# Performance work log

Measured on AMD Instinct MI355X. Metric: run time of the kernel, lower is better.

## Reference

```python
import jax, jax.numpy as jnp
import numpy as np

D_MODEL = 256
D_STATE = 16
D_INNER = 512          # expand=2 * d_model
D_CONV = 4
DT_RANK = 16           # ceil(d_model/16)
B, L = 16, 2048


def setup_inputs() -> dict:
    key = jax.random.key(0)
    ks = jax.random.split(key, 10)
    s = 0.02
    inp = {
        "x": jax.random.normal(ks[0], (B, L, D_MODEL), dtype=jnp.float32),
        "ln_w": jnp.ones((D_MODEL,), jnp.float32),
        "ln_b": jnp.zeros((D_MODEL,), jnp.float32),
        "in_proj_w": jax.random.normal(ks[1], (2 * D_INNER, D_MODEL)) * s,
        "conv_w": jax.random.normal(ks[2], (D_INNER, 1, D_CONV)) * s,
        "conv_b": jnp.zeros((D_INNER,), jnp.float32),
        "x_proj_w": jax.random.normal(ks[3], (DT_RANK + 2 * D_STATE, D_INNER)) * s,
        "dt_proj_w": jax.random.normal(ks[4], (D_INNER, DT_RANK)) * s,
        "dt_proj_b": jax.random.uniform(ks[5], (D_INNER,), minval=-4.0, maxval=-2.0),
        "A_log": jnp.log(jnp.broadcast_to(jnp.arange(1, D_STATE + 1, dtype=jnp.float32), (D_INNER, D_STATE))).copy(),
        "D_param": jnp.ones((D_INNER,), jnp.float32),
        "out_proj_w": jax.random.normal(ks[6], (D_MODEL, D_INNER)) * s,
    }
    return inp


def _layernorm(x, w, b, eps=1e-5):
    mu = jnp.mean(x, axis=-1, keepdims=True)
    var = jnp.var(x, axis=-1, keepdims=True)
    return (x - mu) * jax.lax.rsqrt(var + eps) * w + b


def _mamba(xn, in_proj_w, conv_w, conv_b, x_proj_w, dt_proj_w, dt_proj_b, A_log, D_param, out_proj_w):
    # in_proj -> x, z   (B, L, d_inner) each
    xz = jnp.einsum('bld,ed->ble', xn, in_proj_w)
    x_in, z = jnp.split(xz, 2, axis=-1)

    # depthwise causal conv over L
    xc = jax.lax.conv_general_dilated(
        jnp.transpose(x_in, (0, 2, 1)), conv_w,
        window_strides=(1,), padding=[(D_CONV - 1, 0)],
        feature_group_count=D_INNER,
        dimension_numbers=('NCH', 'OIH', 'NCH')) + conv_b[None, :, None]
    xc = jax.nn.silu(jnp.transpose(xc, (0, 2, 1)))  # (B, L, d_inner)

    # input-dependent dt, B, C
    dbc = jnp.einsum('ble,fe->blf', xc, x_proj_w)  # (B, L, dt_rank + 2N)
    dt = jax.nn.softplus(jnp.einsum('blr,er->ble', dbc[..., :DT_RANK], dt_proj_w) + dt_proj_b)
    Bc = dbc[..., DT_RANK:DT_RANK + D_STATE]   # (B, L, N)
    Cc = dbc[..., DT_RANK + D_STATE:]          # (B, L, N)

    A = -jnp.exp(A_log)  # (d_inner, N)

    def step(h, inputs):
        dt_t, x_t, B_t, C_t = inputs  # (B,e), (B,e), (B,n), (B,n)
        dA = jnp.exp(dt_t[..., None] * A)                      # (B, e, n)
        h = dA * h + dt_t[..., None] * B_t[:, None, :] * x_t[..., None]
        y = jnp.sum(h * C_t[:, None, :], axis=-1)              # (B, e)
        return h, y

    h0 = jnp.zeros((xn.shape[0], D_INNER, D_STATE), xn.dtype)
    seq = (jnp.swapaxes(dt, 0, 1), jnp.swapaxes(xc, 0, 1),
           jnp.swapaxes(Bc, 0, 1), jnp.swapaxes(Cc, 0, 1))
    _, ys = jax.lax.scan(step, h0, seq)
    y = jnp.swapaxes(ys, 0, 1) + D_param * xc                  # (B, L, e)
    y = y * jax.nn.silu(z)
    return jnp.einsum('ble,de->bld', y, out_proj_w)


def reference(x, ln_w, ln_b, in_proj_w, conv_w, conv_b, x_proj_w, dt_proj_w, dt_proj_b, A_log, D_param, out_proj_w):
    xn = _layernorm(x, ln_w, ln_b)
    out = _mamba(xn, in_proj_w, conv_w, conv_b, x_proj_w, dt_proj_w, dt_proj_b, A_log, D_param, out_proj_w)
    return x + out  # dropout is identity in eval
```

## Files before the change

kernel.cpp:

```cpp
#include <hip/hip_runtime.h>
#include <cstdint>

#define DEVI __device__ __forceinline__

typedef __bf16 bf16;
typedef __bf16 bf16x8 __attribute__((ext_vector_type(8)));
typedef __bf16 bf16x4 __attribute__((ext_vector_type(4)));
typedef __bf16 bf16x2 __attribute__((ext_vector_type(2)));
typedef float floatx4 __attribute__((ext_vector_type(4)));
typedef float f32x2 __attribute__((ext_vector_type(2)));

constexpr int BATCH = 16, SEQ = 2048, DM = 256, DI = 512;
constexpr int M = BATCH * SEQ;
constexpr int NC = 128;
constexpr int CL = SEQ / NC;
static_assert(NC * CL == SEQ, "chunking");
constexpr float LOG2E = 1.4426950408889634f;

DEVI void gl2lds16(const void* g, void* l) {
  __builtin_amdgcn_global_load_lds(
      (const __attribute__((address_space(1))) unsigned int*)(uintptr_t)g,
      (__attribute__((address_space(3))) unsigned int*)(unsigned int)(uintptr_t)l,
      16, 0, 0);
}

DEVI float sigmoidf_(float x) { return 1.f / (1.f + __expf(-x)); }
DEVI float exp2_(float x) { return __builtin_amdgcn_exp2f(x); }

DEVI float bflo(unsigned u) { return __uint_as_float(u << 16); }
DEVI float bfhi(unsigned u) { return __uint_as_float(u & 0xFFFF0000u); }
DEVI f32x2 sp2(float v) { f32x2 r; r[0] = v; r[1] = v; return r; }

DEVI void powseq(f32x2 d, f32x2* P) {
  P[0] = d;
  P[1] = d * d;
  P[2] = P[1] * d;
  P[3] = P[1] * P[1];
  P[4] = P[3] * d;
  P[5] = P[3] * P[1];
  P[6] = P[3] * P[2];
  P[7] = P[3] * P[3];
  P[8] = P[7] * d;
  P[9] = P[7] * P[1];
  P[10] = P[7] * P[2];
  P[11] = P[7] * P[3];
  P[12] = P[7] * P[4];
  P[13] = P[7] * P[5];
  P[14] = P[7] * P[6];
  P[15] = P[7] * P[7];
}

__global__ __launch_bounds__(256) void prep_kernel(
    const float* __restrict__ w1, const float* __restrict__ wx,
    const float* __restrict__ wo, const float* __restrict__ alog,
    bf16* __restrict__ w1b, bf16* __restrict__ wxb, bf16* __restrict__ wob,
    float* __restrict__ An, int* __restrict__ flags) {
  constexpr int n1 = 1024 * 256, n2 = 48 * 512, n3 = 256 * 512;
  int i = blockIdx.x * 256 + threadIdx.x;
  if (i < n1) w1b[i] = (bf16)w1[i];
  else if (i < n1 + n2) wxb[i - n1] = (bf16)wx[i - n1];
  else if (i < n1 + n2 + n3) wob[i - n1 - n2] = (bf16)wo[i - n1 - n2];
  else if (i < n1 + n2 + n3 + DI) {
    const int e = i - (n1 + n2 + n3);
    const float a0 = -__expf(alog[e * 16]);
    bool ok = (a0 < 0.f);
#pragma unroll 1
    for (int s = 0; s < 16; s++) {
      const float a = -__expf(alog[e * 16 + s]);
      An[e * 16 + s] = a * LOG2E;
      ok = ok && (__builtin_fabsf(a / a0 - (float)(s + 1)) < 1e-3f);
    }
    flags[e] = ok ? 1 : 0;
  }
}

__global__ __launch_bounds__(256) void ln_kernel(
    const float* __restrict__ x, const float* __restrict__ w,
    const float* __restrict__ b, bf16* __restrict__ xn) {
  const int row = blockIdx.x * 4 + (threadIdx.x >> 6);
  const int lane = threadIdx.x & 63;
  const float4 v = ((const float4*)(x + (size_t)row * DM))[lane];
  float s = v.x + v.y + v.z + v.w;
  float s2 = v.x * v.x + v.y * v.y + v.z * v.z + v.w * v.w;
#pragma unroll
  for (int m = 1; m < 64; m <<= 1) { s += __shfl_xor(s, m); s2 += __shfl_xor(s2, m); }
  const float mu = s * (1.f / DM);
  const float var = s2 * (1.f / DM) - mu * mu;
  const float rs = rsqrtf(var + 1e-5f);
  const float4 wv = ((const float4*)w)[lane];
  const float4 bv = ((const float4*)b)[lane];
  bf16x4 o;
  o[0] = (bf16)((v.x - mu) * rs * wv.x + bv.x);
  o[1] = (bf16)((v.y - mu) * rs * wv.y + bv.y);
  o[2] = (bf16)((v.z - mu) * rs * wv.z + bv.z);
  o[3] = (bf16)((v.w - mu) * rs * wv.w + bv.w);
  *(bf16x4*)(xn + (size_t)row * DM + lane * 4) = o;
}

template <int N, int K, bool OUT_BF16, bool RESID>
__global__ __launch_bounds__(256) void gemm_nt(const bf16* __restrict__ A,
                                               const bf16* __restrict__ W,
                                               void* __restrict__ out,
                                               const float* __restrict__ resid) {
  constexpr int BK = 32;
  constexpr int NB = N / 128;
  constexpr int MT_PER = (M / 128) / 8;
  __shared__ __align__(16) bf16 lA[128 * BK];
  __shared__ __align__(16) bf16 lB[128 * BK];
  const int tid = threadIdx.x;
  const int id = blockIdx.x;
  const int xcd = id & 7;
  const int local = id >> 3;
  const int bm = (xcd * MT_PER + local / NB) * 128;
  const int bn = (local % NB) * 128;
  const int wave = tid >> 6, lane = tid & 63;
  const int wm = (wave >> 1) * 64, wn = (wave & 1) * 64;
  const int q = lane >> 4, r = lane & 15;
  floatx4 acc[4][4] = {};
  const int c0 = wave * 64 + lane;
  const int row0 = c0 >> 2, kp = (c0 & 3) * 8;
  for (int k0 = 0; k0 < K; k0 += BK) {
    gl2lds16(A + (size_t)(bm + row0) * K + k0 + kp, lA + c0 * 8);
    gl2lds16(A + (size_t)(bm + row0 + 64) * K + k0 + kp, lA + (c0 + 256) * 8);
    gl2lds16(W + (size_t)(bn + row0) * K + k0 + kp, lB + c0 * 8);
    gl2lds16(W + (size_t)(bn + row0 + 64) * K + k0 + kp, lB + (c0 + 256) * 8);
    __syncthreads();
    bf16x8 af[4], bfr[4];
#pragma unroll
    for (int i = 0; i < 4; i++) af[i] = *(const bf16x8*)&lA[(wm + i * 16 + r) * BK + q * 8];
#pragma unroll
    for (int j = 0; j < 4; j++) bfr[j] = *(const bf16x8*)&lB[(wn + j * 16 + r) * BK + q * 8];
#pragma unroll
    for (int i = 0; i < 4; i++)
#pragma unroll
      for (int j = 0; j < 4; j++)
        acc[i][j] = __builtin_amdgcn_mfma_f32_16x16x32_bf16(af[i], bfr[j], acc[i][j], 0, 0, 0);
    __syncthreads();
  }
#pragma unroll
  for (int i = 0; i < 4; i++)
#pragma unroll
    for (int j = 0; j < 4; j++)
#pragma unroll
      for (int t = 0; t < 4; t++) {
        const int row = bm + wm + i * 16 + q * 4 + t;
        const int col = bn + wn + j * 16 + r;
        const size_t idx = (size_t)row * N + col;
        float v = acc[i][j][t];
        if constexpr (OUT_BF16) {
          ((bf16*)out)[idx] = (bf16)v;
        } else {
          if constexpr (RESID) v += resid[idx];
          ((float*)out)[idx] = v;
        }
      }
}

__global__ __launch_bounds__(256) void conv_silu(const bf16* __restrict__ xz,
                                                 const float* __restrict__ cw,
                                                 const float* __restrict__ cb,
                                                 bf16* __restrict__ xc) {
  const int tid = threadIdx.x;
  const int e2 = tid * 2;
  const int p0 = blockIdx.x * 8;
  const int b = blockIdx.y;
  const float4 w0 = ((const float4*)cw)[e2];
  const float4 w1 = ((const float4*)cw)[e2 + 1];
  const float2 bias = *(const float2*)(cb + e2);
  float xa[11], xb_[11];
#pragma unroll
  for (int j = 0; j < 11; j++) {
    const int pos = p0 - 3 + j;
    float fa = 0.f, fb = 0.f;
    if (pos >= 0) {
      const unsigned u = *(const unsigned*)(xz + ((size_t)b * SEQ + pos) * 1024 + e2);
      fa = __uint_as_float(u << 16);
      fb = __uint_as_float(u & 0xFFFF0000u);
    }
    xa[j] = fa; xb_[j] = fb;
  }
#pragma unroll
  for (int k = 0; k < 8; k++) {
    const float a0 = bias.x + xa[k] * w0.x + xa[k + 1] * w0.y + xa[k + 2] * w0.z + xa[k + 3] * w0.w;
    const float a1 = bias.y + xb_[k] * w1.x + xb_[k + 1] * w1.y + xb_[k + 2] * w1.z + xb_[k + 3] * w1.w;
    bf16x2 o;
    o[0] = (bf16)(a0 * sigmoidf_(a0));
    o[1] = (bf16)(a1 * sigmoidf_(a1));
    *(bf16x2*)(xc + ((size_t)b * SEQ + p0 + k) * DI + e2) = o;
  }
}

__global__ __launch_bounds__(256) void gemm_xproj(const bf16* __restrict__ A,
                                                  const bf16* __restrict__ W,
                                                  float* __restrict__ out) {
  constexpr int K = DI;
  __shared__ __align__(16) bf16 lW[48 * K];
  __shared__ __align__(16) bf16 lA[64 * 32];
  const int tid = threadIdx.x;
  const int wave = tid >> 6, lane = tid & 63;
  const int bm = blockIdx.x * 64;
  const int q = lane >> 4, r = lane & 15;
#pragma unroll
  for (int rd = 0; rd < 12; rd++) {
    const int c = rd * 256 + tid;
    gl2lds16((const char*)W + (size_t)c * 16, (char*)lW + (size_t)c * 16);
  }
  const int row0 = tid >> 2, kp = (tid & 3) * 8;
  const int wm = wave * 16;
  floatx4 acc[3] = {};
  for (int k0 = 0; k0 < K; k0 += 32) {
    gl2lds16(A + (size_t)(bm + row0) * K + k0 + kp, lA + tid * 8);
    __syncthreads();
    bf16x8 af = *(const bf16x8*)&lA[(wm + r) * 32 + q * 8];
#pragma unroll
    for (int j = 0; j < 3; j++) {
      const bf16x8 bfr = *(const bf16x8*)&lW[(j * 16 + r) * K + k0 + q * 8];
      acc[j] = __builtin_amdgcn_mfma_f32_16x16x32_bf16(af, bfr, acc[j], 0, 0, 0);
    }
    __syncthreads();
  }
#pragma unroll
  for (int j = 0; j < 3; j++)
#pragma unroll
    for (int t = 0; t < 4; t++)
      out[(size_t)(bm + wm + q * 4 + t) * 48 + j * 16 + r] = acc[j][t];
}

__global__ __launch_bounds__(256) void dtproj_kernel(const float* __restrict__ dbc,
                                                     const float* __restrict__ dtw,
                                                     const float* __restrict__ dtb,
                                                     bf16* __restrict__ dt) {
  __shared__ __align__(16) float sd[64 * 16];
  const int tid = threadIdx.x;
  const int p0 = blockIdx.x * 64;
  const int e = blockIdx.y * 256 + tid;
  {
    const int rowi = tid >> 2, coli = (tid & 3) * 4;
    *(float4*)&sd[rowi * 16 + coli] = *(const float4*)(dbc + (size_t)(p0 + rowi) * 48 + coli);
  }
  float w[16];
#pragma unroll
  for (int s = 0; s < 16; s += 4) {
    float4 t4 = *(const float4*)(dtw + (size_t)e * 16 + s);
    w[s] = t4.x; w[s + 1] = t4.y; w[s + 2] = t4.z; w[s + 3] = t4.w;
  }
  const float bias = dtb[e];
  __syncthreads();
  for (int p = 0; p < 64; p++) {
    float s = bias;
#pragma unroll
    for (int r2 = 0; r2 < 16; r2++) s += sd[p * 16 + r2] * w[r2];
    const float sp = (s > 15.f) ? s : __logf(1.f + __expf(s));
    dt[(size_t)(p0 + p) * DI + e] = (bf16)sp;
  }
}

__global__ __launch_bounds__(256) void scan_pass1(const bf16* __restrict__ dt,
                                                  const bf16* __restrict__ xc,
                                                  const float* __restrict__ dbc,
                                                  const float* __restrict__ An,
                                                  const int* __restrict__ flags,
                                                  float* __restrict__ U,
                                                  float* __restrict__ SD) {
  __shared__ __align__(16) float sbc[CL * 16];
  const int tid = threadIdx.x;
  const int e2 = tid * 2;
  const int ch = blockIdx.x, b = blockIdx.y;
  const size_t posBase = (size_t)b * SEQ + (size_t)ch * CL;
  if (tid < CL * 4) {
    const int il = tid >> 2, f = (tid & 3) * 4;
    gl2lds16(dbc + (posBase + il) * 48 + 16 + f, (char*)sbc + tid * 16);
  }
  const int2 fl = *(const int2*)(flags + e2);
  const int fast = fl.x & fl.y;
  f32x2 h[16];
#pragma unroll
  for (int s = 0; s < 16; s++) { h[s][0] = 0.f; h[s][1] = 0.f; }
  f32x2 sdt2; sdt2[0] = 0.f; sdt2[1] = 0.f;
  f32x2 A02; A02[0] = An[(size_t)e2 * 16]; A02[1] = An[(size_t)e2 * 16 + 16];
  float Aa[16], Ab[16];
  if (!fast) {
#pragma unroll
    for (int s = 0; s < 16; s += 4) {
      float4 a4 = *(const float4*)(An + (size_t)e2 * 16 + s);
      Aa[s] = a4.x; Aa[s + 1] = a4.y; Aa[s + 2] = a4.z; Aa[s + 3] = a4.w;
      float4 b4 = *(const float4*)(An + (size_t)e2 * 16 + 16 + s);
      Ab[s] = b4.x; Ab[s + 1] = b4.y; Ab[s + 2] = b4.z; Ab[s + 3] = b4.w;
    }
  }
  const char* pdt = (const char*)(dt + posBase * DI + e2);
  const char* pxc = (const char*)(xc + posBase * DI + e2);
  unsigned ud = *(const unsigned*)pdt;
  unsigned ux = *(const unsigned*)pxc;
  __syncthreads();
  if (fast) {
#pragma unroll 1
    for (int il = 0; il < CL; il++) {
      const int np = (il + 1 < CL) ? (il + 1) : il;
      const unsigned nud = *(const unsigned*)(pdt + (size_t)np * DI * 2);
      const unsigned nux = *(const unsigned*)(pxc + (size_t)np * DI * 2);
      f32x2 dt2; dt2[0] = bflo(ud); dt2[1] = bfhi(ud);
      f32x2 xv2; xv2[0] = bflo(ux); xv2[1] = bfhi(ux);
      const f32x2 dtx2 = dt2 * xv2;
      sdt2 = sdt2 + dt2;
      const f32x2 t = dt2 * A02;
      f32x2 d; d[0] = exp2_(t[0]); d[1] = exp2_(t[1]);
      f32x2 P[16];
      powseq(d, P);
      const float4* bb = (const float4*)(sbc + il * 16);
#pragma unroll
      for (int g = 0; g < 4; g++) {
        const float4 B4 = bb[g];
        h[4 * g + 0] = P[4 * g + 0] * h[4 * g + 0] + dtx2 * sp2(B4.x);
        h[4 * g + 1] = P[4 * g + 1] * h[4 * g + 1] + dtx2 * sp2(B4.y);
        h[4 * g + 2] = P[4 * g + 2] * h[4 * g + 2] + dtx2 * sp2(B4.z);
        h[4 * g + 3] = P[4 * g + 3] * h[4 * g + 3] + dtx2 * sp2(B4.w);
      }
      ud = nud; ux = nux;
    }
  } else {
#pragma unroll 1
    for (int il = 0; il < CL; il++) {
      const int np = (il + 1 < CL) ? (il + 1) : il;
      const unsigned nud = *(const unsigned*)(pdt + (size_t)np * DI * 2);
      const unsigned nux = *(const unsigned*)(pxc + (size_t)np * DI * 2);
      const float dta = bflo(ud), dtb_v = bfhi(ud);
      const float xa = bflo(ux), xb = bfhi(ux);
      const float dtxa = dta * xa, dtxb = dtb_v * xb;
      sdt2[0] += dta; sdt2[1] += dtb_v;
      const float* bc = sbc + il * 16;
#pragma unroll
      for (int s = 0; s < 16; s++) {
        const float bv = bc[s];
        h[s][0] = exp2_(dta * Aa[s]) * h[s][0] + dtxa * bv;
        h[s][1] = exp2_(dtb_v * Ab[s]) * h[s][1] + dtxb * bv;
      }
      ud = nud; ux = nux;
    }
  }
  float* up = U + ((size_t)(b * NC + ch) * DI + e2) * 16;
#pragma unroll
  for (int i = 0; i < 4; i++) {
    float4 o; o.x = h[4 * i][0]; o.y = h[4 * i + 1][0]; o.z = h[4 * i + 2][0]; o.w = h[4 * i + 3][0];
    ((float4*)up)[i] = o;
  }
#pragma unroll
  for (int i = 0; i < 4; i++) {
    float4 o; o.x = h[4 * i][1]; o.y = h[4 * i + 1][1]; o.z = h[4 * i + 2][1]; o.w = h[4 * i + 3][1];
    ((float4*)up)[4 + i] = o;
  }
  float2 sdo; sdo.x = sdt2[0]; sdo.y = sdt2[1];
  *(float2*)(SD + (size_t)(b * NC + ch) * DI + e2) = sdo;
}

__global__ __launch_bounds__(256) void scan_pass2(const float* __restrict__ SD,
                                                  float* U,
                                                  const float* __restrict__ An) {
  const int t = blockIdx.x * 256 + threadIdx.x;
  const int s = t & 15;
  const int e = (t >> 4) & (DI - 1);
  const int b = t >> 13;
  const float Av = An[e * 16 + s];
  const float* sdp = SD + (size_t)b * NC * DI + e;
  float* up = U + ((size_t)b * NC * DI + e) * 16 + s;
  float sA_[16], uA_[16], sB_[16], uB_[16];
#pragma unroll
  for (int j = 0; j < 16; j++) {
    sA_[j] = sdp[(size_t)j * DI];
    uA_[j] = up[(size_t)j * DI * 16];
  }
  float h = 0.f;
#pragma unroll 1
  for (int c0 = 0; c0 < NC; c0 += 32) {
#pragma unroll
    for (int j = 0; j < 16; j++) {
      sB_[j] = sdp[(size_t)(c0 + 16 + j) * DI];
      uB_[j] = up[(size_t)(c0 + 16 + j) * DI * 16];
    }
#pragma unroll
    for (int j = 0; j < 16; j++) {
      const float h0 = h;
      h = exp2_(Av * sA_[j]) * h0 + uA_[j];
      up[(size_t)(c0 + j) * DI * 16] = h0;
    }
    const int nn = (c0 + 32 < NC) ? (c0 + 32) : (NC - 16);
#pragma unroll
    for (int j = 0; j < 16; j++) {
      sA_[j] = sdp[(size_t)(nn + j) * DI];
      uA_[j] = up[(size_t)(nn + j) * DI * 16];
    }
#pragma unroll
    for (int j = 0; j < 16; j++) {
      const float h0 = h;
      h = exp2_(Av * sB_[j]) * h0 + uB_[j];
      up[(size_t)(c0 + 16 + j) * DI * 16] = h0;
    }
  }
}

__global__ __launch_bounds__(256) void scan_pass3(const bf16* __restrict__ dt,
                                                  const bf16* __restrict__ xc,
                                                  const bf16* __restrict__ xz,
                                                  const float* __restrict__ dbc,
                                                  const float* __restrict__ An,
                                                  const int* __restrict__ flags,
                                                  const float* __restrict__ H0,
                                                  const float* __restrict__ Dp,
                                                  bf16* __restrict__ yg) {
  __shared__ __align__(16) float sbc[CL * 32];
  const int tid = threadIdx.x;
  const int e2 = tid * 2;
  const int ch = blockIdx.x, b = blockIdx.y;
  const size_t posBase = (size_t)b * SEQ + (size_t)ch * CL;
  if (tid < CL * 8) {
    const int il = tid >> 3, f = (tid & 7) * 4;
    gl2lds16(dbc + (posBase + il) * 48 + 16 + f, (char*)sbc + tid * 16);
  }
  const int2 fl = *(const int2*)(flags + e2);
  const int fast = fl.x & fl.y;
  f32x2 h[16];
  const float* hp = H0 + ((size_t)(b * NC + ch) * DI + e2) * 16;
#pragma unroll
  for (int i = 0; i < 4; i++) {
    const float4 h4 = ((const float4*)hp)[i];
    h[4 * i][0] = h4.x; h[4 * i + 1][0] = h4.y; h[4 * i + 2][0] = h4.z; h[4 * i + 3][0] = h4.w;
  }
#pragma unroll
  for (int i = 0; i < 4; i++) {
    const float4 h4 = ((const float4*)hp)[4 + i];
    h[4 * i][1] = h4.x; h[4 * i + 1][1] = h4.y; h[4 * i + 2][1] = h4.z; h[4 * i + 3][1] = h4.w;
  }
  const float2 Dv = *(const float2*)(Dp + e2);
  f32x2 Dv2; Dv2[0] = Dv.x; Dv2[1] = Dv.y;
  f32x2 A02; A02[0] = An[(size_t)e2 * 16]; A02[1] = An[(size_t)e2 * 16 + 16];
  float Aa[16], Ab[16];
  if (!fast) {
#pragma unroll
    for (int s = 0; s < 16; s += 4) {
      float4 a4 = *(const float4*)(An + (size_t)e2 * 16 + s);
      Aa[s] = a4.x; Aa[s + 1] = a4.y; Aa[s + 2] = a4.z; Aa[s + 3] = a4.w;
      float4 b4 = *(const float4*)(An + (size_t)e2 * 16 + 16 + s);
      Ab[s] = b4.x; Ab[s + 1] = b4.y; Ab[s + 2] = b4.z; Ab[s + 3] = b4.w;
    }
  }
  const char* pdt = (const char*)(dt + posBase * DI + e2);
  const char* pxc = (const char*)(xc + posBase * DI + e2);
  const char* pxz = (const char*)(xz + posBase * 1024 + DI + e2);
  unsigned ud = *(const unsigned*)pdt;
  unsigned ux = *(const unsigned*)pxc;
  unsigned uz = *(const unsigned*)pxz;
  __syncthreads();
  if (fast) {
#pragma unroll 1
    for (int il = 0; il < CL; il++) {
      const int np = (il + 1 < CL) ? (il + 1) : il;
      const unsigned nud = *(const unsigned*)(pdt + (size_t)np * DI * 2);
      const unsigned nux = *(const unsigned*)(pxc + (size_t)np * DI * 2);
      const unsigned nuz = *(const unsigned*)(pxz + (size_t)np * 1024 * 2);
      const size_t pos = posBase + il;
      f32x2 dt2; dt2[0] = bflo(ud); dt2[1] = bfhi(ud);
      f32x2 xv2; xv2[0] = bflo(ux); xv2[1] = bfhi(ux);
      f32x2 z2; z2[0] = bflo(uz); z2[1] = bfhi(uz);
      const f32x2 dtx2 = dt2 * xv2;
      const f32x2 t = dt2 * A02;
      f32x2 d; d[0] = exp2_(t[0]); d[1] = exp2_(t[1]);
      f32x2 P[16];
      powseq(d, P);
      const float4* bb = (const float4*)(sbc + il * 32);
      f32x2 Yv[4];
#pragma unroll
      for (int g = 0; g < 4; g++) { Yv[g][0] = 0.f; Yv[g][1] = 0.f; }
#pragma unroll
      for (int g = 0; g < 4; g++) {
        const float4 B4 = bb[g];
        const float4 C4 = bb[4 + g];
        h[4 * g + 0] = P[4 * g + 0] * h[4 * g + 0] + dtx2 * sp2(B4.x);
        Yv[g] = Yv[g] + h[4 * g + 0] * sp2(C4.x);
        h[4 * g + 1] = P[4 * g + 1] * h[4 * g + 1] + dtx2 * sp2(B4.y);
        Yv[g] = Yv[g] + h[4 * g + 1] * sp2(C4.y);
        h[4 * g + 2] = P[4 * g + 2] * h[4 * g + 2] + dtx2 * sp2(B4.z);
        Yv[g] = Yv[g] + h[4 * g + 2] * sp2(C4.z);
        h[4 * g + 3] = P[4 * g + 3] * h[4 * g + 3] + dtx2 * sp2(B4.w);
        Yv[g] = Yv[g] + h[4 * g + 3] * sp2(C4.w);
      }
      const f32x2 Ys = (Yv[0] + Yv[1]) + (Yv[2] + Yv[3]);
      f32x2 gz; gz[0] = z2[0] * sigmoidf_(z2[0]); gz[1] = z2[1] * sigmoidf_(z2[1]);
      const f32x2 yv2 = (Ys + Dv2 * xv2) * gz;
      bf16x2 o; o[0] = (bf16)yv2[0]; o[1] = (bf16)yv2[1];
      *(bf16x2*)(yg + pos * DI + e2) = o;
      ud = nud; ux = nux; uz = nuz;
    }
  } else {
#pragma unroll 1
    for (int il = 0; il < CL; il++) {
      const int np = (il + 1 < CL) ? (il + 1) : il;
      const unsigned nud = *(const unsigned*)(pdt + (size_t)np * DI * 2);
      const unsigned nux = *(const unsigned*)(pxc + (size_t)np * DI * 2);
      const unsigned nuz = *(const unsigned*)(pxz + (size_t)np * 1024 * 2);
      const size_t pos = posBase + il;
      const float dta = bflo(ud), dtb_v = bfhi(ud);
      const float xa = bflo(ux), xb = bfhi(ux);
      const float za = bflo(uz), zb = bfhi(uz);
      const float dtxa = dta * xa, dtxb = dtb_v * xb;
      const float* bc = sbc + il * 32;
      float ya = 0.f, yb = 0.f;
#pragma unroll
      for (int s = 0; s < 16; s++) {
        const float bv = bc[s], cv = bc[16 + s];
        const float ha = exp2_(dta * Aa[s]) * h[s][0] + dtxa * bv;
        const float hb = exp2_(dtb_v * Ab[s]) * h[s][1] + dtxb * bv;
        h[s][0] = ha; h[s][1] = hb;
        ya += ha * cv; yb += hb * cv;
      }
      const float yva = (ya + Dv.x * xa) * za * sigmoidf_(za);
      const float yvb = (yb + Dv.y * xb) * zb * sigmoidf_(zb);
      bf16x2 o; o[0] = (bf16)yva; o[1] = (bf16)yvb;
      *(bf16x2*)(yg + pos * DI + e2) = o;
      ud = nud; ux = nux; uz = nuz;
    }
  }
}

extern "C" void kernel_launch(void* const* d_in, const int* in_sizes, int n_in,
                              void* d_out, int out_size, void* d_ws, size_t ws_size,
                              hipStream_t stream) {
  const float* x = (const float*)d_in[0];
  const float* ln_w = (const float*)d_in[1];
  const float* ln_b = (const float*)d_in[2];
  const float* w_in = (const float*)d_in[3];
  const float* conv_w = (const float*)d_in[4];
  const float* conv_b = (const float*)d_in[5];
  const float* w_x = (const float*)d_in[6];
  const float* w_dt = (const float*)d_in[7];
  const float* b_dt = (const float*)d_in[8];
  const float* a_log = (const float*)d_in[9];
  const float* d_par = (const float*)d_in[10];
  const float* w_out = (const float*)d_in[11];

  char* ws = (char*)d_ws;
  size_t off = 0;
  auto alloc = [&](size_t bytes) {
    void* p = ws + off;
    off = (off + bytes + 255) & ~(size_t)255;
    return p;
  };
  bf16* xzb = (bf16*)alloc((size_t)M * 1024 * 2);
  bf16* xcb = (bf16*)alloc((size_t)M * DI * 2);
  float* dbc = (float*)alloc((size_t)M * 48 * 4);
  bf16* dtb_ = (bf16*)alloc((size_t)M * DI * 2);
  bf16* ygb = (bf16*)alloc((size_t)M * DI * 2);
  float* U = (float*)alloc((size_t)BATCH * NC * DI * 16 * 4);
  bf16* xn = (bf16*)U;
  float* SD = (float*)alloc((size_t)BATCH * NC * DI * 4);
  bf16* w1b = (bf16*)alloc(1024 * 256 * 2);
  bf16* wxb = (bf16*)alloc(48 * 512 * 2);
  bf16* wob = (bf16*)alloc(256 * 512 * 2);
  float* An = (float*)alloc(512 * 16 * 4);
  int* flags = (int*)alloc(512 * 4);

  constexpr int prep_n = 1024 * 256 + 48 * 512 + 256 * 512 + DI;
  prep_kernel<<<dim3((prep_n + 255) / 256), dim3(256), 0, stream>>>(w_in, w_x, w_out, a_log, w1b, wxb, wob, An, flags);
  ln_kernel<<<dim3(M / 4), dim3(256), 0, stream>>>(x, ln_w, ln_b, xn);
  gemm_nt<1024, 256, true, false><<<dim3((M / 128) * 8), dim3(256), 0, stream>>>(xn, w1b, (void*)xzb, nullptr);
  conv_silu<<<dim3(SEQ / 8, BATCH), dim3(256), 0, stream>>>(xzb, conv_w, conv_b, xcb);
  gemm_xproj<<<dim3(M / 64), dim3(256), 0, stream>>>(xcb, wxb, dbc);
  dtproj_kernel<<<dim3(M / 64, 2), dim3(256), 0, stream>>>(dbc, w_dt, b_dt, dtb_);
  scan_pass1<<<dim3(NC, BATCH), dim3(256), 0, stream>>>(dtb_, xcb, dbc, An, flags, U, SD);
  scan_pass2<<<dim3(BATCH * DI * 16 / 256), dim3(256), 0, stream>>>(SD, U, An);
  scan_pass3<<<dim3(NC, BATCH), dim3(256), 0, stream>>>(dtb_, xcb, xzb, dbc, An, flags, U, d_par, ygb);
  gemm_nt<256, 512, false, true><<<dim3((M / 128) * 2), dim3(256), 0, stream>>>(ygb, wob, d_out, x);
}
```

Measured before the change: 328.2 us.

## Fuse dt projection and softplus into scan passes, halve chunk count

Removes the separate dtproj kernel and its bf16 dt buffer. Each scan pass now recomputes dt per timestep from the staged dbc rows using per-thread dt_proj weights and bias. Chunk count drops from 128 to 64, and pass1 double-buffers xc rows into LDS in sub-chunks of 8. This saves a full M×512 write and two reads of dt in exchange for about 32 extra FMAs plus a softplus per channel pair per step in both passes. Halving the chunk count also cuts the number of blocks, which lowers parallelism.

```diff
diff --git a/kernel.cpp b/kernel.cpp
--- a/kernel.cpp
+++ b/kernel.cpp
@@ -12,8 +12,10 @@
 
 constexpr int BATCH = 16, SEQ = 2048, DM = 256, DI = 512;
 constexpr int M = BATCH * SEQ;
-constexpr int NC = 128;
+constexpr int NC = 64;
 constexpr int CL = SEQ / NC;
+constexpr int SC = 8;
+constexpr int NSC = CL / SC;
 static_assert(NC * CL == SEQ, "chunking");
 constexpr float LOG2E = 1.4426950408889634f;
 
@@ -30,6 +32,25 @@
 DEVI float bflo(unsigned u) { return __uint_as_float(u << 16); }
 DEVI float bfhi(unsigned u) { return __uint_as_float(u & 0xFFFF0000u); }
 DEVI f32x2 sp2(float v) { f32x2 r; r[0] = v; r[1] = v; return r; }
+
+DEVI float softplus_(float s) { return (s > 15.f) ? s : __logf(1.f + __expf(s)); }
+
+DEVI float2 dt_pair(const float* dr, const float* w0, const float* w1, float2 bias) {
+  float a0 = bias.x, a1 = 0.f, a2 = 0.f, a3 = 0.f;
+  float b0 = bias.y, b1 = 0.f, b2 = 0.f, b3 = 0.f;
+#pragma unroll
+  for (int r = 0; r < 4; r++) {
+    const float4 v = ((const float4*)dr)[r];
+    a0 += v.x * w0[4 * r + 0]; a1 += v.y * w0[4 * r + 1];
+    a2 += v.z * w0[4 * r + 2]; a3 += v.w * w0[4 * r + 3];
+    b0 += v.x * w1[4 * r + 0]; b1 += v.y * w1[4 * r + 1];
+    b2 += v.z * w1[4 * r + 2]; b3 += v.w * w1[4 * r + 3];
+  }
+  float2 r2;
+  r2.x = softplus_((a0 + a1) + (a2 + a3));
+  r2.y = softplus_((b0 + b1) + (b2 + b3));
+  return r2;
+}
 
 DEVI void powseq(f32x2 d, f32x2* P) {
   P[0] = d;
@@ -48,6 +69,11 @@
   P[13] = P[7] * P[5];
   P[14] = P[7] * P[6];
   P[15] = P[7] * P[7];
+}
+
+DEVI void stage_rows(const bf16* src, bf16* dst, int tid) {
+  gl2lds16((const char*)src + tid * 16, (char*)dst + tid * 16);
+  gl2lds16((const char*)src + tid * 16 + 4096, (char*)dst + tid * 16 + 4096);
 }
 
 __global__ __launch_bounds__(256) void prep_kernel(
@@ -226,51 +252,25 @@
       out[(size_t)(bm + wm + q * 4 + t) * 48 + j * 16 + r] = acc[j][t];
 }
 
-__global__ __launch_bounds__(256) void dtproj_kernel(const float* __restrict__ dbc,
-                                                     const float* __restrict__ dtw,
-                                                     const float* __restrict__ dtb,
-                                                     bf16* __restrict__ dt) {
-  __shared__ __align__(16) float sd[64 * 16];
-  const int tid = threadIdx.x;
-  const int p0 = blockIdx.x * 64;
-  const int e = blockIdx.y * 256 + tid;
-  {
-    const int rowi = tid >> 2, coli = (tid & 3) * 4;
-    *(float4*)&sd[rowi * 16 + coli] = *(const float4*)(dbc + (size_t)(p0 + rowi) * 48 + coli);
-  }
-  float w[16];
-#pragma unroll
-  for (int s = 0; s < 16; s += 4) {
-    float4 t4 = *(const float4*)(dtw + (size_t)e * 16 + s);
-    w[s] = t4.x; w[s + 1] = t4.y; w[s + 2] = t4.z; w[s + 3] = t4.w;
-  }
-  const float bias = dtb[e];
-  __syncthreads();
-  for (int p = 0; p < 64; p++) {
-    float s = bias;
-#pragma unroll
-    for (int r2 = 0; r2 < 16; r2++) s += sd[p * 16 + r2] * w[r2];
-    const float sp = (s > 15.f) ? s : __logf(1.f + __expf(s));
-    dt[(size_t)(p0 + p) * DI + e] = (bf16)sp;
-  }
-}
-
-__global__ __launch_bounds__(256) void scan_pass1(const bf16* __restrict__ dt,
-                                                  const bf16* __restrict__ xc,
+__global__ __launch_bounds__(256) void scan_pass1(const bf16* __restrict__ xc,
                                                   const float* __restrict__ dbc,
                                                   const float* __restrict__ An,
                                                   const int* __restrict__ flags,
+                                                  const float* __restrict__ dtw,
+                                                  const float* __restrict__ dtb,
                                                   float* __restrict__ U,
                                                   float* __restrict__ SD) {
-  __shared__ __align__(16) float sbc[CL * 16];
+  __shared__ __align__(16) float sbc[CL * 32];
+  __shared__ __align__(16) bf16 sxc_[2][SC * DI];
   const int tid = threadIdx.x;
   const int e2 = tid * 2;
   const int ch = blockIdx.x, b = blockIdx.y;
   const size_t posBase = (size_t)b * SEQ + (size_t)ch * CL;
-  if (tid < CL * 4) {
-    const int il = tid >> 2, f = (tid & 3) * 4;
-    gl2lds16(dbc + (posBase + il) * 48 + 16 + f, (char*)sbc + tid * 16);
-  }
+  {
+    const int il = tid >> 3, f = (tid & 7) * 4;
+    gl2lds16(dbc + (posBase + il) * 48 + f, (char*)sbc + tid * 16);
+  }
+  stage_rows(xc + posBase * DI, sxc_[0], tid);
   const int2 fl = *(const int2*)(flags + e2);
   const int fast = fl.x & fl.y;
   f32x2 h[16];
@@ -288,55 +288,72 @@
       Ab[s] = b4.x; Ab[s + 1] = b4.y; Ab[s + 2] = b4.z; Ab[s + 3] = b4.w;
     }
   }
-  const char* pdt = (const char*)(dt + posBase * DI + e2);
-  const char* pxc = (const char*)(xc + posBase * DI + e2);
-  unsigned ud = *(const unsigned*)pdt;
-  unsigned ux = *(const unsigned*)pxc;
+  float w0_[16], w1_[16];
+#pragma unroll
+  for (int r = 0; r < 16; r += 4) {
+    float4 t0 = *(const float4*)(dtw + (size_t)e2 * 16 + r);
+    w0_[r] = t0.x; w0_[r + 1] = t0.y; w0_[r + 2] = t0.z; w0_[r + 3] = t0.w;
+    float4 t1 = *(const float4*)(dtw + (size_t)(e2 + 1) * 16 + r);
+    w1_[r] = t1.x; w1_[r + 1] = t1.y; w1_[r + 2] = t1.z; w1_[r + 3] = t1.w;
+  }
+  const float2 bias = *(const float2*)(dtb + e2);
   __syncthreads();
-  if (fast) {
+  float2 dtc = dt_pair(sbc, w0_, w1_, bias);
 #pragma unroll 1
-    for (int il = 0; il < CL; il++) {
-      const int np = (il + 1 < CL) ? (il + 1) : il;
-      const unsigned nud = *(const unsigned*)(pdt + (size_t)np * DI * 2);
-      const unsigned nux = *(const unsigned*)(pxc + (size_t)np * DI * 2);
-      f32x2 dt2; dt2[0] = bflo(ud); dt2[1] = bfhi(ud);
-      f32x2 xv2; xv2[0] = bflo(ux); xv2[1] = bfhi(ux);
-      const f32x2 dtx2 = dt2 * xv2;
-      sdt2 = sdt2 + dt2;
-      const f32x2 t = dt2 * A02;
-      f32x2 d; d[0] = exp2_(t[0]); d[1] = exp2_(t[1]);
-      f32x2 P[16];
-      powseq(d, P);
-      const float4* bb = (const float4*)(sbc + il * 16);
-#pragma unroll
-      for (int g = 0; g < 4; g++) {
-        const float4 B4 = bb[g];
-        h[4 * g + 0] = P[4 * g + 0] * h[4 * g + 0] + dtx2 * sp2(B4.x);
-        h[4 * g + 1] = P[4 * g + 1] * h[4 * g + 1] + dtx2 * sp2(B4.y);
-        h[4 * g + 2] = P[4 * g + 2] * h[4 * g + 2] + dtx2 * sp2(B4.z);
-        h[4 * g + 3] = P[4 * g + 3] * h[4 * g + 3] + dtx2 * sp2(B4.w);
+  for (int sc = 0; sc < NSC; sc++) {
+    const int cb = sc & 1;
+    if (sc + 1 < NSC)
+      stage_rows(xc + (posBase + (sc + 1) * SC) * DI, sxc_[cb ^ 1], tid);
+    const char* sxcb = (const char*)sxc_[cb];
+    const int tid4 = tid * 4;
+    if (fast) {
+#pragma unroll 2
+      for (int il = 0; il < SC; il++) {
+        const int ig = sc * SC + il;
+        const int ng = (ig + 1 < CL) ? (ig + 1) : ig;
+        const float2 dtn = dt_pair(sbc + ng * 32, w0_, w1_, bias);
+        const unsigned ux = *(const unsigned*)(sxcb + il * 1024 + tid4);
+        f32x2 dt2; dt2[0] = dtc.x; dt2[1] = dtc.y;
+        f32x2 xv2; xv2[0] = bflo(ux); xv2[1] = bfhi(ux);
+        const f32x2 dtx2 = dt2 * xv2;
+        sdt2 = sdt2 + dt2;
+        const f32x2 t = dt2 * A02;
+        f32x2 d; d[0] = exp2_(t[0]); d[1] = exp2_(t[1]);
+        f32x2 P[16];
+        powseq(d, P);
+        const float4* bb = (const float4*)(sbc + ig * 32 + 16);
+#pragma unroll
+        for (int g = 0; g < 4; g++) {
+          const float4 B4 = bb[g];
+          h[4 * g + 0] = P[4 * g + 0] * h[4 * g + 0] + dtx2 * sp2(B4.x);
+          h[4 * g + 1] = P[4 * g + 1] * h[4 * g + 1] + dtx2 * sp2(B4.y);
+          h[4 * g + 2] = P[4 * g + 2] * h[4 * g + 2] + dtx2 * sp2(B4.z);
+          h[4 * g + 3] = P[4 * g + 3] * h[4 * g + 3] + dtx2 * sp2(B4.w);
+        }
+        dtc = dtn;
       }
-      ud = nud; ux = nux;
-    }
-  } else {
-#pragma unroll 1
-    for (int il = 0; il < CL; il++) {
-      const int np = (il + 1 < CL) ? (il + 1) : il;
-      const unsigned nud = *(const unsigned*)(pdt + (size_t)np * DI * 2);
-      const unsigned nux = *(const unsigned*)(pxc + (size_t)np * DI * 2);
-      const float dta = bflo(ud), dtb_v = bfhi(ud);
-      const float xa = bflo(ux), xb = bfhi(ux);
-      const float dtxa = dta * xa, dtxb = dtb_v * xb;
-      sdt2[0] += dta; sdt2[1] += dtb_v;
-      const float* bc = sbc + il * 16;
-#pragma unroll
-      for (int s = 0; s < 16; s++) {
-        const float bv = bc[s];
-        h[s][0] = exp2_(dta * Aa[s]) * h[s][0] + dtxa * bv;
-        h[s][1] = exp2_(dtb_v * Ab[s]) * h[s][1] + dtxb * bv;
+    } else {
+#pragma unroll 2
+      for (int il = 0; il < SC; il++) {
+        const int ig = sc * SC + il;
+        const int ng = (ig + 1 < CL) ? (ig + 1) : ig;
+        const float2 dtn = dt_pair(sbc + ng * 32, w0_, w1_, bias);
+        const unsigned ux = *(const unsigned*)(sxcb + il * 1024 + tid4);
+        const float dta = dtc.x, dtb_v = dtc.y;
+        const float xa = bflo(ux), xb = bfhi(ux);
+        const float dtxa = dta * xa, dtxb = dtb_v * xb;
+        sdt2[0] += dta; sdt2[1] += dtb_v;
+        const float* bc = sbc + ig * 32 + 16;
+#pragma unroll
+        for (int s = 0; s < 16; s++) {
+          const float bv = bc[s];
+          h[s][0] = exp2_(dta * Aa[s]) * h[s][0] + dtxa * bv;
+          h[s][1] = exp2_(dtb_v * Ab[s]) * h[s][1] + dtxb * bv;
+        }
+        dtc = dtn;
       }
-      ud = nud; ux = nux;
-    }
+    }
+    __syncthreads();
   }
   float* up = U + ((size_t)(b * NC + ch) * DI + e2) * 16;
 #pragma unroll
@@ -398,24 +415,24 @@
   }
 }
 
-__global__ __launch_bounds__(256) void scan_pass3(const bf16* __restrict__ dt,
-                                                  const bf16* __restrict__ xc,
+__global__ __launch_bounds__(256) void scan_pass3(const bf16* __restrict__ xc,
                                                   const bf16* __restrict__ xz,
                                                   const float* __restrict__ dbc,
                                                   const float* __restrict__ An,
                                                   const int* __restrict__ flags,
                                                   const float* __restrict__ H0,
                                                   const float* __restrict__ Dp,
+                                                  const float* __restrict__ dtw,
+                                                  const float* __restrict__ dtb,
                                                   bf16* __restrict__ yg) {
-  __shared__ __align__(16) float sbc[CL * 32];
+  __shared__ __align__(16) float sbc[CL * 48];
   const int tid = threadIdx.x;
   const int e2 = tid * 2;
   const int ch = blockIdx.x, b = blockIdx.y;
   const size_t posBase = (size_t)b * SEQ + (size_t)ch * CL;
-  if (tid < CL * 8) {
-    const int il = tid >> 3, f = (tid & 7) * 4;
-    gl2lds16(dbc + (posBase + il) * 48 + 16 + f, (char*)sbc + tid * 16);
-  }
+  gl2lds16(dbc + posBase * 48 + (size_t)tid * 4, (char*)sbc + tid * 16);
+  if (tid < 128)
+    gl2lds16(dbc + posBase * 48 + 1024 + (size_t)tid * 4, (char*)sbc + 4096 + tid * 16);
   const int2 fl = *(const int2*)(flags + e2);
   const int fast = fl.x & fl.y;
   f32x2 h[16];
@@ -443,22 +460,30 @@
       Ab[s] = b4.x; Ab[s + 1] = b4.y; Ab[s + 2] = b4.z; Ab[s + 3] = b4.w;
     }
   }
-  const char* pdt = (const char*)(dt + posBase * DI + e2);
+  float w0_[16], w1_[16];
+#pragma unroll
+  for (int r = 0; r < 16; r += 4) {
+    float4 t0 = *(const float4*)(dtw + (size_t)e2 * 16 + r);
+    w0_[r] = t0.x; w0_[r + 1] = t0.y; w0_[r + 2] = t0.z; w0_[r + 3] = t0.w;
+    float4 t1 = *(const float4*)(dtw + (size_t)(e2 + 1) * 16 + r);
+    w1_[r] = t1.x; w1_[r + 1] = t1.y; w1_[r + 2] = t1.z; w1_[r + 3] = t1.w;
+  }
+  const float2 bias = *(const float2*)(dtb + e2);
   const char* pxc = (const char*)(xc + posBase * DI + e2);
   const char* pxz = (const char*)(xz + posBase * 1024 + DI + e2);
-  unsigned ud = *(const unsigned*)pdt;
   unsigned ux = *(const unsigned*)pxc;
   unsigned uz = *(const unsigned*)pxz;
   __syncthreads();
+  float2 dtc = dt_pair(sbc, w0_, w1_, bias);
   if (fast) {
 #pragma unroll 1
     for (int il = 0; il < CL; il++) {
       const int np = (il + 1 < CL) ? (il + 1) : il;
-      const unsigned nud = *(const unsigned*)(pdt + (size_t)np * DI * 2);
       const unsigned nux = *(const unsigned*)(pxc + (size_t)np * DI * 2);
       const unsigned nuz = *(const unsigned*)(pxz + (size_t)np * 1024 * 2);
+      const float2 dtn = dt_pair(sbc + np * 48, w0_, w1_, bias);
       const size_t pos = posBase + il;
-      f32x2 dt2; dt2[0] = bflo(ud); dt2[1] = bfhi(ud);
+      f32x2 dt2; dt2[0] = dtc.x; dt2[1] = dtc.y;
       f32x2 xv2; xv2[0] = bflo(ux); xv2[1] = bfhi(ux);
       f32x2 z2; z2[0] = bflo(uz); z2[1] = bfhi(uz);
       const f32x2 dtx2 = dt2 * xv2;
@@ -466,7 +491,7 @@
       f32x2 d; d[0] = exp2_(t[0]); d[1] = exp2_(t[1]);
       f32x2 P[16];
       powseq(d, P);
-      const float4* bb = (const float4*)(sbc + il * 32);
+      const float4* bb = (const float4*)(sbc + il * 48 + 16);
       f32x2 Yv[4];
 #pragma unroll
       for (int g = 0; g < 4; g++) { Yv[g][0] = 0.f; Yv[g][1] = 0.f; }
@@ -485,24 +510,25 @@
       }
       const f32x2 Ys = (Yv[0] + Yv[1]) + (Yv[2] + Yv[3]);
       f32x2 gz; gz[0] = z2[0] * sigmoidf_(z2[0]); gz[1] = z2[1] * sigmoidf_(z2[1]);
-      const f32x2 yv2 = (Ys + Dv2 * xv2) * gz;
+      const f32x2 xvv = dt2 * sp2(0.f) + xv2;
+      const f32x2 yv2 = (Ys + Dv2 * xvv) * gz;
       bf16x2 o; o[0] = (bf16)yv2[0]; o[1] = (bf16)yv2[1];
       *(bf16x2*)(yg + pos * DI + e2) = o;
-      ud = nud; ux = nux; uz = nuz;
+      ux = nux; uz = nuz; dtc = dtn;
     }
   } else {
 #pragma unroll 1
     for (int il = 0; il < CL; il++) {
       const int np = (il + 1 < CL) ? (il + 1) : il;
-      const unsigned nud = *(const unsigned*)(pdt + (size_t)np * DI * 2);
       const unsigned nux = *(const unsigned*)(pxc + (size_t)np * DI * 2);
       const unsigned nuz = *(const unsigned*)(pxz + (size_t)np * 1024 * 2);
+      const float2 dtn = dt_pair(sbc + np * 48, w0_, w1_, bias);
       const size_t pos = posBase + il;
-      const float dta = bflo(ud), dtb_v = bfhi(ud);
+      const float dta = dtc.x, dtb_v = dtc.y;
       const float xa = bflo(ux), xb = bfhi(ux);
       const float za = bflo(uz), zb = bfhi(uz);
       const float dtxa = dta * xa, dtxb = dtb_v * xb;
-      const float* bc = sbc + il * 32;
+      const float* bc = sbc + il * 48 + 16;
       float ya = 0.f, yb = 0.f;
 #pragma unroll
       for (int s = 0; s < 16; s++) {
@@ -516,7 +542,7 @@
       const float yvb = (yb + Dv.y * xb) * zb * sigmoidf_(zb);
       bf16x2 o; o[0] = (bf16)yva; o[1] = (bf16)yvb;
       *(bf16x2*)(yg + pos * DI + e2) = o;
-      ud = nud; ux = nux; uz = nuz;
+      ux = nux; uz = nuz; dtc = dtn;
     }
   }
 }
@@ -547,7 +573,6 @@
   bf16* xzb = (bf16*)alloc((size_t)M * 1024 * 2);
   bf16* xcb = (bf16*)alloc((size_t)M * DI * 2);
   float* dbc = (float*)alloc((size_t)M * 48 * 4);
-  bf16* dtb_ = (bf16*)alloc((size_t)M * DI * 2);
   bf16* ygb = (bf16*)alloc((size_t)M * DI * 2);
   float* U = (float*)alloc((size_t)BATCH * NC * DI * 16 * 4);
   bf16* xn = (bf16*)U;
@@ -564,9 +589,8 @@
   gemm_nt<1024, 256, true, false><<<dim3((M / 128) * 8), dim3(256), 0, stream>>>(xn, w1b, (void*)xzb, nullptr);
   conv_silu<<<dim3(SEQ / 8, BATCH), dim3(256), 0, stream>>>(xzb, conv_w, conv_b, xcb);
   gemm_xproj<<<dim3(M / 64), dim3(256), 0, stream>>>(xcb, wxb, dbc);
-  dtproj_kernel<<<dim3(M / 64, 2), dim3(256), 0, stream>>>(dbc, w_dt, b_dt, dtb_);
-  scan_pass1<<<dim3(NC, BATCH), dim3(256), 0, stream>>>(dtb_, xcb, dbc, An, flags, U, SD);
+  scan_pass1<<<dim3(NC, BATCH), dim3(256), 0, stream>>>(xcb, dbc, An, flags, w_dt, b_dt, U, SD);
   scan_pass2<<<dim3(BATCH * DI * 16 / 256), dim3(256), 0, stream>>>(SD, U, An);
-  scan_pass3<<<dim3(NC, BATCH), dim3(256), 0, stream>>>(dtb_, xcb, xzb, dbc, An, flags, U, d_par, ygb);
+  scan_pass3<<<dim3(NC, BATCH), dim3(256), 0, stream>>>(xcb, xzb, dbc, An, flags, U, d_par, w_dt, b_dt, ygb);
   gemm_nt<256, 512, false, true><<<dim3((M / 128) * 2), dim3(256), 0, stream>>>(ygb, wob, d_out, x);
 }
```

Measured after the change: 298.8 us. 9.0% less time.
